# Kernel optimization log

Hardware: AMD Instinct MI355X
Metric: run time of the kernel (lower is better)

The kernel has to match this reference:

```python
import jax, jax.numpy as jnp
import numpy as np

NUM_HEADS = 8
NEG_INF = -1e30


def _within_bucket_rank(idx):
    # idx: [U] int32 bucket ids; returns occurrence count of each id among earlier positions
    U = idx.shape[0]
    order = jnp.argsort(idx, stable=True)
    sv = idx[order]
    pos = jnp.arange(U, dtype=jnp.int32)
    is_start = jnp.concatenate([jnp.ones((1,), bool), sv[1:] != sv[:-1]])
    start = jax.lax.cummax(jnp.where(is_start, pos, 0))
    rank = pos - start
    return jnp.zeros(U, jnp.int32).at[order].set(rank)


def setup_inputs() -> dict:
    key = jax.random.key(0)
    ks = jax.random.split(key, 10)
    B, U, G, E = 8, 16384, 64, 128
    lin = jnp.linspace(0.0, 1.0, G)
    gx, gy = jnp.meshgrid(lin, lin, indexing='ij')
    xc_on_grid = jnp.broadcast_to(jnp.stack([gx, gy], -1), (B, G, G, 2)).astype(jnp.float32)
    s = 0.02
    return {
        'xc_off_grid': jax.random.uniform(ks[0], (B, U, 2), jnp.float32),
        'xc_on_grid': xc_on_grid,
        'zc_off_grid': jax.random.normal(ks[1], (B, U, E), jnp.float32),
        'zc_on_grid': jax.random.normal(ks[2], (B, G, G, E), jnp.float32),
        'latents': jax.random.normal(ks[3], (G * G, E), jnp.float32),
        'fake_embedding': jax.random.normal(ks[4], (E,), jnp.float32),
        'Wq': jax.random.normal(ks[5], (E, E), jnp.float32) * s,
        'Wk': jax.random.normal(ks[6], (E, E), jnp.float32) * s,
        'Wv': jax.random.normal(ks[7], (E, E), jnp.float32) * s,
        'Wo': jax.random.normal(ks[8], (E, E), jnp.float32) * s,
        'ignore_on_grid': 0,
    }


def _bucketize(xc_off_grid, xc_on_grid):
    # returns nearest flat grid index per off-grid point, shape [B, U] int32
    B = xc_off_grid.shape[0]
    dims = xc_on_grid.shape[1:-1]
    S = int(np.prod(dims))
    grid_shape = jnp.asarray(dims, jnp.float32)
    x_on = xc_on_grid.reshape(B, S, -1)
    xmin = x_on.min(axis=(0, 1))
    xmax = x_on.max(axis=(0, 1))
    spacing = (xmax - xmin) / (grid_shape - 1.0)
    nm = jnp.floor((xc_off_grid - xmin + spacing / 2) / spacing)
    nm = jnp.clip(nm, 0.0, grid_shape - 1.0)
    # strides as in the original: flip(cumprod([1, *dims])[:-1])
    strides = np.flip(np.cumprod(np.concatenate([[1], np.asarray(dims)]))[:-1]).astype(np.float32)
    return (nm * jnp.asarray(strides)).sum(-1).astype(jnp.int32)


def _mhca(latents_q, kv, valid, Wq, Wk, Wv, Wo):
    # latents_q: [N,1,E], kv: [N,P,E], valid: [N,P] bool
    N, P, E = kv.shape
    H, Dh = NUM_HEADS, E // NUM_HEADS
    q = (latents_q @ Wq).reshape(N, 1, H, Dh)
    k = (kv @ Wk).reshape(N, P, H, Dh)
    v = (kv @ Wv).reshape(N, P, H, Dh)
    scores = jnp.einsum('nqhd,nkhd->nhqk', q, k) / jnp.sqrt(jnp.asarray(Dh, q.dtype))
    scores = jnp.where(valid[:, None, None, :], scores, NEG_INF)
    attn = jax.nn.softmax(scores, axis=-1)
    out = jnp.einsum('nhqk,nkhd->nqhd', attn, v).reshape(N, 1, E)
    return out @ Wo


def reference(xc_off_grid, xc_on_grid, zc_off_grid, zc_on_grid, latents, fake_embedding, Wq, Wk, Wv, Wo, ignore_on_grid):
    B, U, E = zc_off_grid.shape
    dims = xc_on_grid.shape[1:-1]
    S = int(np.prod(dims))
    z_on = zc_on_grid.reshape(B, S, E)

    nearest_idx = _bucketize(xc_off_grid, xc_on_grid)          # [B, U]
    cumcount = jax.vmap(_within_bucket_rank)(nearest_idx)       # [B, U]
    flat_seg = (nearest_idx + jnp.arange(B, dtype=jnp.int32)[:, None] * S).reshape(-1)
    counts = jax.ops.segment_sum(jnp.ones(B * U, jnp.int32), flat_seg, num_segments=B * S)
    max_patch = int(jax.device_get(counts.max())) + 1           # +1 slot for on-grid/fake token

    # ragged scatter of off-grid tokens into padded per-bucket buffer
    grid_stacked = jnp.zeros((B * S, max_patch, E), zc_off_grid.dtype)
    grid_stacked = grid_stacked.at[flat_seg, cumcount.reshape(-1)].set(zc_off_grid.reshape(B * U, E))
    if ignore_on_grid:
        last = jnp.broadcast_to(fake_embedding, (B * S, E))
    else:
        last = z_on.reshape(B * S, E)
    grid_stacked = grid_stacked.at[:, -1].set(last)

    slot = jnp.arange(max_patch)
    valid = (slot[None, :] < counts[:, None]) | (slot[None, :] == max_patch - 1)  # [B*S, P]

    lat = jnp.broadcast_to(latents[None], (B, S, E)).reshape(B * S, 1, E)
    zc = _mhca(lat, grid_stacked, valid, Wq, Wk, Wv, Wo)        # [B*S, 1, E]
    return zc.reshape(B, *dims, E)
```

## Files before the change

kernel.cpp:

```cpp
#include <hip/hip_runtime.h>
#include <hip/hip_bf16.h>
#include <math.h>

namespace {
constexpr int B_  = 8;
constexpr int U_  = 16384;
constexpr int S_  = 4096;
constexpr int E_  = 128;
constexpr int NTOK  = B_ * U_;
constexpr int NCELL = B_ * S_;
constexpr int FUSED_GRID = 768;
constexpr int CAP = 32;
constexpr int SWZ2 = 2 * 16384;
}

typedef __attribute__((ext_vector_type(8))) short bf16x8;
typedef __attribute__((ext_vector_type(4))) float f32x4;

__device__ inline unsigned short bf16rne(float x) {
  unsigned u = __float_as_uint(x);
  u = u + 0x7fffu + ((u >> 16) & 1u);
  return (unsigned short)(u >> 16);
}

__device__ inline bf16x8 pack8(float4 a, float4 b) {
  union { __hip_bfloat162 h; unsigned int u; } q0, q1, q2, q3;
  q0.h = __float22bfloat162_rn(make_float2(a.x, a.y));
  q1.h = __float22bfloat162_rn(make_float2(a.z, a.w));
  q2.h = __float22bfloat162_rn(make_float2(b.x, b.y));
  q3.h = __float22bfloat162_rn(make_float2(b.z, b.w));
  union { unsigned int u[4]; bf16x8 v; } r;
  r.u[0] = q0.u; r.u[1] = q1.u; r.u[2] = q2.u; r.u[3] = q3.u;
  return r.v;
}

__global__ __launch_bounds__(1024, 4) void setup_kernel(
    const float* __restrict__ Wq, const float* __restrict__ Wv,
    const float* __restrict__ Wo,
    const float* __restrict__ latents, const float* __restrict__ xc_off,
    unsigned short* __restrict__ Wsw, float* __restrict__ Qp,
    int* __restrict__ cnt, int* __restrict__ sorted) {
  const int tid = threadIdx.x;

  if (blockIdx.x < 16) {
    __shared__ __align__(16) unsigned short wq[16384];
    for (int i = tid; i < 16384; i += 1024) {
      const int k = i >> 7, n = i & 127;
      wq[(((k >> 3) * 128 + n) << 3) + (k & 7)] = bf16rne(Wq[i]);
    }
    __syncthreads();

    const int wave = tid >> 6, lane = tid & 63;
    const int c = lane & 15, g = lane >> 4;
    const int t0w = blockIdx.x * 256 + wave * 16;

    f32x4 acc[8];
#pragma unroll
    for (int i = 0; i < 8; ++i) acc[i] = {0.f, 0.f, 0.f, 0.f};

    const float* arow = latents + (size_t)(t0w + c) * E_ + g * 8;
    const bf16x8* bq = (const bf16x8*)wq;
#pragma unroll
    for (int ks = 0; ks < 4; ++ks) {
      float4 a0 = *(const float4*)(arow + ks * 32);
      float4 a1 = *(const float4*)(arow + ks * 32 + 4);
      bf16x8 af = pack8(a0, a1);
      const int bo = (ks * 4 + g) * 128 + c;
#pragma unroll
      for (int nt = 0; nt < 8; ++nt)
        acc[nt] = __builtin_amdgcn_mfma_f32_16x16x32_bf16(af, bq[bo + nt * 16], acc[nt], 0, 0, 0);
    }
#pragma unroll
    for (int nt = 0; nt < 8; ++nt)
#pragma unroll
      for (int r = 0; r < 4; ++r)
        Qp[(size_t)(t0w + g * 4 + r) * E_ + c * 8 + nt] = acc[nt][r] * 0.25f;
  } else {
    const int base = (blockIdx.x - 16) * 1024 + tid;
    const int stride = 240 * 1024;
    for (int i = base; i < SWZ2 + NTOK; i += stride) {
      if (i < SWZ2) {
        const int w = i >> 14, e = i & 16383;
        const int k = e >> 7, n = e & 127;
        const float* src = (w == 0) ? Wv : Wo;
        Wsw[w * 16384 + (((k >> 3) * 128 + n) << 3) + (k & 7)] = bf16rne(src[e]);
      } else {
        const int tok = i - SWZ2;
        const int b = tok >> 14;
        const float sp = 1.0f / 63.0f;
        const float half = sp * 0.5f;
        const float x0 = xc_off[(size_t)tok * 2 + 0];
        const float x1 = xc_off[(size_t)tok * 2 + 1];
        float n0 = floorf((x0 - 0.0f + half) / sp);
        float n1 = floorf((x1 - 0.0f + half) / sp);
        n0 = fminf(fmaxf(n0, 0.0f), 63.0f);
        n1 = fminf(fmaxf(n1, 0.0f), 63.0f);
        const int seg = b * S_ + (int)(n0 * 64.0f + n1);
        const int rank = atomicAdd(&cnt[seg], 1);
        if (rank < CAP) sorted[seg * CAP + rank] = tok;
      }
    }
  }
}

__global__ __launch_bounds__(256) void qk_table(
    const float* __restrict__ Wk, const float* __restrict__ Qp,
    unsigned short* __restrict__ QKt) {
  __shared__ float wkl[128 * 129];
  __shared__ float qls[16 * 128];
  const int tid = threadIdx.x;
  const int s0 = blockIdx.x * 16;

  for (int i = tid; i < 16384; i += 256)
    wkl[(i >> 7) * 129 + (i & 127)] = Wk[i];
  for (int i = tid; i < 2048; i += 256) {
    const int sl = i >> 7, idx = i & 127;
    qls[sl * 128 + (idx & 7) * 16 + (idx >> 3)] = Qp[(size_t)(s0 + sl) * E_ + idx];
  }
  __syncthreads();

  const int e = tid & 127, half = tid >> 7;
#pragma unroll
  for (int h = 0; h < 8; ++h) {
    float wr[16];
#pragma unroll
    for (int j = 0; j < 16; ++j) wr[j] = wkl[e * 129 + h * 16 + j];
#pragma unroll
    for (int cl = 0; cl < 8; ++cl) {
      const int sl = half * 8 + cl;
      float acc = 0.f;
#pragma unroll
      for (int j = 0; j < 16; ++j)
        acc = fmaf(wr[j], qls[sl * 128 + h * 16 + j], acc);
      QKt[(size_t)(s0 + sl) * 1024 + (e >> 3) * 64 + h * 8 + (e & 7)] = bf16rne(acc);
    }
  }
}

__global__ __launch_bounds__(512, 6) void fused_cells(
    const float* __restrict__ zc_off, const float* __restrict__ zc_on,
    const float* __restrict__ fake, const int* __restrict__ ignore_flag,
    const unsigned short* __restrict__ Wv_sw,
    const unsigned short* __restrict__ QKt, const int* __restrict__ cnt,
    const int* __restrict__ sorted, float* __restrict__ out) {
  __shared__ __align__(16) unsigned short wv[16384];
  __shared__ float wbuf[8][16][9];
  const int tid = threadIdx.x;
  {
    const uint4* sv = (const uint4*)Wv_sw;
    uint4* dv = (uint4*)wv;
#pragma unroll
    for (int i = 0; i < 4; ++i) dv[i * 512 + tid] = sv[i * 512 + tid];
  }
  const int ign = *ignore_flag;
  __syncthreads();

  const int wave = tid >> 6, lane = tid & 63;
  const int c = lane & 15, g = lane >> 4;
  const bf16x8* bv = (const bf16x8*)wv;

  for (int grp = blockIdx.x; grp < NCELL / 8; grp += FUSED_GRID) {
    const int cell = grp * 8 + wave;
    const int s = cell & (S_ - 1);
    const int base = cell * CAP;
    const int n_off = min(cnt[cell], CAP);
    const bf16x8* bqk = (const bf16x8*)(QKt + (size_t)s * 1024);

    float num_acc[8], den_acc[8];
#pragma unroll
    for (int i = 0; i < 8; ++i) { num_acc[i] = 0.f; den_acc[i] = 0.f; }

    const int chunks = (n_off + 16) >> 4;

    for (int ch = 0; ch < chunks; ++ch) {
      const int idx = ch * 16 + c;
      const float* arow;
      if (idx < n_off)       arow = zc_off + (size_t)sorted[base + idx] * E_;
      else if (idx == n_off) arow = ign ? fake : (zc_on + (size_t)cell * E_);
      else                   arow = zc_on;
      arow += g * 8;

      bf16x8 af[4];
#pragma unroll
      for (int ks = 0; ks < 4; ++ks) {
        float4 a0 = *(const float4*)(arow + ks * 32);
        float4 a1 = *(const float4*)(arow + ks * 32 + 4);
        af[ks] = pack8(a0, a1);
      }

      f32x4 aS = {0.f, 0.f, 0.f, 0.f};
#pragma unroll
      for (int ks = 0; ks < 4; ++ks)
        aS = __builtin_amdgcn_mfma_f32_16x16x32_bf16(af[ks], bqk[(ks * 4 + g) * 8 + (c & 7)], aS, 0, 0, 0);

      if (c < 8) {
#pragma unroll
        for (int r = 0; r < 4; ++r) {
          const int t = g * 4 + r;
          wbuf[wave][t][c] = (ch * 16 + t <= n_off) ? __expf(aS[r]) : 0.f;
        }
      }

#pragma unroll 2
      for (int h = 0; h < 8; ++h) {
        float wr[4];
#pragma unroll
        for (int r = 0; r < 4; ++r) wr[r] = wbuf[wave][g * 4 + r][h];

        const int bo = g * 128 + c + h * 16;
        f32x4 aV = {0.f, 0.f, 0.f, 0.f};
#pragma unroll
        for (int ks = 0; ks < 4; ++ks)
          aV = __builtin_amdgcn_mfma_f32_16x16x32_bf16(af[ks], bv[bo + ks * 512], aV, 0, 0, 0);

        float sv = 0.f, sd = 0.f;
#pragma unroll
        for (int r = 0; r < 4; ++r) { sv = fmaf(wr[r], aV[r], sv); sd += wr[r]; }
        num_acc[h] += sv;
        den_acc[h] += sd;
      }
    }

#pragma unroll
    for (int i = 0; i < 8; ++i) {
      num_acc[i] += __shfl_xor(num_acc[i], 16, 64);
      num_acc[i] += __shfl_xor(num_acc[i], 32, 64);
      den_acc[i] += __shfl_xor(den_acc[i], 16, 64);
      den_acc[i] += __shfl_xor(den_acc[i], 32, 64);
    }
#pragma unroll
    for (int b = 0; b < 2; ++b) {
      const int nt = 2 * g + b;
      out[(size_t)cell * E_ + nt * 16 + c] = num_acc[nt] / den_acc[nt];
    }
  }
}

__global__ __launch_bounds__(512, 4) void finalize_mfma(
    const unsigned short* __restrict__ Wo_sw, float* __restrict__ out) {
  __shared__ __align__(16) unsigned short wo[16384];
  const int tid = threadIdx.x;
  {
    const uint4* s = (const uint4*)Wo_sw;
    uint4* d = (uint4*)wo;
#pragma unroll
    for (int i = 0; i < 4; ++i) d[i * 512 + tid] = s[i * 512 + tid];
  }
  __syncthreads();

  const int wave = tid >> 6, lane = tid & 63;
  const int c = lane & 15, g = lane >> 4;
  const int t0w = blockIdx.x * 128 + wave * 16;

  f32x4 acc[8];
#pragma unroll
  for (int i = 0; i < 8; ++i) acc[i] = {0.f, 0.f, 0.f, 0.f};

  const float* nrow = out + (size_t)(t0w + c) * E_ + g * 8;
  const bf16x8* bo_ = (const bf16x8*)wo;
#pragma unroll
  for (int ks = 0; ks < 4; ++ks) {
    float4 a0 = *(const float4*)(nrow + ks * 32);
    float4 a1 = *(const float4*)(nrow + ks * 32 + 4);
    bf16x8 af = pack8(a0, a1);
    const int bofs = (ks * 4 + g) * 128 + c;
#pragma unroll
    for (int nt = 0; nt < 8; ++nt)
      acc[nt] = __builtin_amdgcn_mfma_f32_16x16x32_bf16(af, bo_[bofs + nt * 16], acc[nt], 0, 0, 0);
  }
#pragma unroll
  for (int nt = 0; nt < 8; ++nt)
#pragma unroll
    for (int r = 0; r < 4; ++r)
      out[(size_t)(t0w + g * 4 + r) * E_ + nt * 16 + c] = acc[nt][r];
}

extern "C" void kernel_launch(void* const* d_in, const int* in_sizes, int n_in,
                              void* d_out, int out_size, void* d_ws, size_t ws_size,
                              hipStream_t stream) {
  const float* xc_off  = (const float*)d_in[0];
  const float* zc_off  = (const float*)d_in[2];
  const float* zc_on   = (const float*)d_in[3];
  const float* latents = (const float*)d_in[4];
  const float* fake    = (const float*)d_in[5];
  const float* Wq      = (const float*)d_in[6];
  const float* Wk      = (const float*)d_in[7];
  const float* Wv      = (const float*)d_in[8];
  const float* Wo      = (const float*)d_in[9];
  const int*   ignore  = (const int*)d_in[10];

  float* out = (float*)d_out;

  float* Qp = (float*)d_ws;
  unsigned short* Wsw = (unsigned short*)(Qp + (size_t)S_ * E_);
  unsigned short* QKt = Wsw + SWZ2;
  int* cnt    = (int*)(QKt + (size_t)S_ * 1024);
  int* sorted = cnt + NCELL;
  unsigned short* Wv_sw = Wsw;
  unsigned short* Wo_sw = Wsw + 16384;

  hipMemsetAsync(cnt, 0, NCELL * sizeof(int), stream);
  setup_kernel<<<256, 1024, 0, stream>>>(Wq, Wv, Wo, latents, xc_off,
                                         Wsw, Qp, cnt, sorted);
  qk_table<<<S_ / 16, 256, 0, stream>>>(Wk, Qp, QKt);
  fused_cells<<<FUSED_GRID, 512, 0, stream>>>(zc_off, zc_on, fake, ignore,
                                              Wv_sw, QKt, cnt, sorted, out);
  finalize_mfma<<<NCELL / 128, 512, 0, stream>>>(Wo_sw, out);
}
```

Measured before the change: 215.3 us.

## Fuse QK table computation into setup kernel and retune fused_cells grid

Removes the separate qk_table kernel by computing the Q projection into shared memory and then the per-head Wk·Q table inside 128 blocks of the setup kernel. This drops one launch and the Qp round trip through global memory. The bucketing work is now spread over 128 blocks instead of 240. Separately, the fused_cells grid grows from 768 to 1024 blocks and its launch-bounds occupancy hint drops from 6 to 4. The setup kernel's shared-memory footprint grows to about 114 KB per block, which limits residency and may slow the bucketing blocks that share that kernel.

```diff
diff --git a/kernel.cpp b/kernel.cpp
--- a/kernel.cpp
+++ b/kernel.cpp
@@ -9,7 +9,7 @@
 constexpr int E_  = 128;
 constexpr int NTOK  = B_ * U_;
 constexpr int NCELL = B_ * S_;
-constexpr int FUSED_GRID = 768;
+constexpr int FUSED_GRID = 1024;
 constexpr int CAP = 32;
 constexpr int SWZ2 = 2 * 16384;
 }
@@ -35,49 +35,66 @@
 }
 
 __global__ __launch_bounds__(1024, 4) void setup_kernel(
-    const float* __restrict__ Wq, const float* __restrict__ Wv,
-    const float* __restrict__ Wo,
+    const float* __restrict__ Wq, const float* __restrict__ Wk,
+    const float* __restrict__ Wv, const float* __restrict__ Wo,
     const float* __restrict__ latents, const float* __restrict__ xc_off,
-    unsigned short* __restrict__ Wsw, float* __restrict__ Qp,
+    unsigned short* __restrict__ Wsw, unsigned short* __restrict__ QKt,
     int* __restrict__ cnt, int* __restrict__ sorted) {
   const int tid = threadIdx.x;
 
-  if (blockIdx.x < 16) {
+  if (blockIdx.x < 128) {
     __shared__ __align__(16) unsigned short wq[16384];
+    __shared__ float wkt[128 * 129];
+    __shared__ float qbuf[32 * 128];
+    const int s0 = blockIdx.x * 32;
+
     for (int i = tid; i < 16384; i += 1024) {
       const int k = i >> 7, n = i & 127;
       wq[(((k >> 3) * 128 + n) << 3) + (k & 7)] = bf16rne(Wq[i]);
+      wkt[(i & 127) * 129 + (i >> 7)] = Wk[i];
     }
     __syncthreads();
 
     const int wave = tid >> 6, lane = tid & 63;
     const int c = lane & 15, g = lane >> 4;
-    const int t0w = blockIdx.x * 256 + wave * 16;
-
-    f32x4 acc[8];
-#pragma unroll
-    for (int i = 0; i < 8; ++i) acc[i] = {0.f, 0.f, 0.f, 0.f};
-
-    const float* arow = latents + (size_t)(t0w + c) * E_ + g * 8;
-    const bf16x8* bq = (const bf16x8*)wq;
-#pragma unroll
-    for (int ks = 0; ks < 4; ++ks) {
-      float4 a0 = *(const float4*)(arow + ks * 32);
-      float4 a1 = *(const float4*)(arow + ks * 32 + 4);
-      bf16x8 af = pack8(a0, a1);
-      const int bo = (ks * 4 + g) * 128 + c;
+    if (wave < 2) {
+      const int t0w = s0 + wave * 16;
+      f32x4 acc[8];
+#pragma unroll
+      for (int i = 0; i < 8; ++i) acc[i] = {0.f, 0.f, 0.f, 0.f};
+      const float* arow = latents + (size_t)(t0w + c) * E_ + g * 8;
+      const bf16x8* bq = (const bf16x8*)wq;
+#pragma unroll
+      for (int ks = 0; ks < 4; ++ks) {
+        float4 a0 = *(const float4*)(arow + ks * 32);
+        float4 a1 = *(const float4*)(arow + ks * 32 + 4);
+        bf16x8 af = pack8(a0, a1);
+        const int bo = (ks * 4 + g) * 128 + c;
+#pragma unroll
+        for (int nt = 0; nt < 8; ++nt)
+          acc[nt] = __builtin_amdgcn_mfma_f32_16x16x32_bf16(af, bq[bo + nt * 16], acc[nt], 0, 0, 0);
+      }
 #pragma unroll
       for (int nt = 0; nt < 8; ++nt)
-        acc[nt] = __builtin_amdgcn_mfma_f32_16x16x32_bf16(af, bq[bo + nt * 16], acc[nt], 0, 0, 0);
-    }
-#pragma unroll
-    for (int nt = 0; nt < 8; ++nt)
-#pragma unroll
-      for (int r = 0; r < 4; ++r)
-        Qp[(size_t)(t0w + g * 4 + r) * E_ + c * 8 + nt] = acc[nt][r] * 0.25f;
+#pragma unroll
+        for (int r = 0; r < 4; ++r)
+          qbuf[(wave * 16 + g * 4 + r) * 128 + nt * 16 + c] = acc[nt][r] * 0.25f;
+    }
+    __syncthreads();
+
+#pragma unroll
+    for (int k = 0; k < 32; ++k) {
+      const int o = k * 1024 + tid;
+      const int e = o & 127, h = (o >> 7) & 7, sl = o >> 10;
+      float acc = 0.f;
+#pragma unroll
+      for (int j = 0; j < 16; ++j)
+        acc = fmaf(wkt[(h * 16 + j) * 129 + e], qbuf[sl * 128 + h * 16 + j], acc);
+      QKt[(size_t)(s0 + sl) * 1024 + (e >> 3) * 64 + h * 8 + (e & 7)] = bf16rne(acc);
+    }
   } else {
-    const int base = (blockIdx.x - 16) * 1024 + tid;
-    const int stride = 240 * 1024;
+    const int base = (blockIdx.x - 128) * 1024 + tid;
+    const int stride = 128 * 1024;
     for (int i = base; i < SWZ2 + NTOK; i += stride) {
       if (i < SWZ2) {
         const int w = i >> 14, e = i & 16383;
@@ -103,41 +120,7 @@
   }
 }
 
-__global__ __launch_bounds__(256) void qk_table(
-    const float* __restrict__ Wk, const float* __restrict__ Qp,
-    unsigned short* __restrict__ QKt) {
-  __shared__ float wkl[128 * 129];
-  __shared__ float qls[16 * 128];
-  const int tid = threadIdx.x;
-  const int s0 = blockIdx.x * 16;
-
-  for (int i = tid; i < 16384; i += 256)
-    wkl[(i >> 7) * 129 + (i & 127)] = Wk[i];
-  for (int i = tid; i < 2048; i += 256) {
-    const int sl = i >> 7, idx = i & 127;
-    qls[sl * 128 + (idx & 7) * 16 + (idx >> 3)] = Qp[(size_t)(s0 + sl) * E_ + idx];
-  }
-  __syncthreads();
-
-  const int e = tid & 127, half = tid >> 7;
-#pragma unroll
-  for (int h = 0; h < 8; ++h) {
-    float wr[16];
-#pragma unroll
-    for (int j = 0; j < 16; ++j) wr[j] = wkl[e * 129 + h * 16 + j];
-#pragma unroll
-    for (int cl = 0; cl < 8; ++cl) {
-      const int sl = half * 8 + cl;
-      float acc = 0.f;
-#pragma unroll
-      for (int j = 0; j < 16; ++j)
-        acc = fmaf(wr[j], qls[sl * 128 + h * 16 + j], acc);
-      QKt[(size_t)(s0 + sl) * 1024 + (e >> 3) * 64 + h * 8 + (e & 7)] = bf16rne(acc);
-    }
-  }
-}
-
-__global__ __launch_bounds__(512, 6) void fused_cells(
+__global__ __launch_bounds__(512, 4) void fused_cells(
     const float* __restrict__ zc_off, const float* __restrict__ zc_on,
     const float* __restrict__ fake, const int* __restrict__ ignore_flag,
     const unsigned short* __restrict__ Wv_sw,
@@ -291,18 +274,16 @@
 
   float* out = (float*)d_out;
 
-  float* Qp = (float*)d_ws;
-  unsigned short* Wsw = (unsigned short*)(Qp + (size_t)S_ * E_);
-  unsigned short* QKt = Wsw + SWZ2;
-  int* cnt    = (int*)(QKt + (size_t)S_ * 1024);
+  unsigned short* QKt = (unsigned short*)d_ws;
+  unsigned short* Wsw = QKt + (size_t)S_ * 1024;
+  int* cnt    = (int*)(Wsw + SWZ2);
   int* sorted = cnt + NCELL;
   unsigned short* Wv_sw = Wsw;
   unsigned short* Wo_sw = Wsw + 16384;
 
   hipMemsetAsync(cnt, 0, NCELL * sizeof(int), stream);
-  setup_kernel<<<256, 1024, 0, stream>>>(Wq, Wv, Wo, latents, xc_off,
-                                         Wsw, Qp, cnt, sorted);
-  qk_table<<<S_ / 16, 256, 0, stream>>>(Wk, Qp, QKt);
+  setup_kernel<<<256, 1024, 0, stream>>>(Wq, Wk, Wv, Wo, latents, xc_off,
+                                         Wsw, QKt, cnt, sorted);
   fused_cells<<<FUSED_GRID, 512, 0, stream>>>(zc_off, zc_on, fake, ignore,
                                               Wv_sw, QKt, cnt, sorted, out);
   finalize_mfma<<<NCELL / 128, 512, 0, stream>>>(Wo_sw, out);
```

Result: faster. 186.5 us (-13.4%).
